# Optimization experiments

Measured on AMD Instinct MI355X. Metric: run time of the kernel, lower is better.

The kernel has to match this reference:

```python
import jax, jax.numpy as jnp
import numpy as np

B, T, D = 4, 4096, 1024
EPS = 1e-5


def _layernorm(x, w):
    mu = jnp.mean(x, axis=-1, keepdims=True)
    var = jnp.var(x, axis=-1, keepdims=True)
    return (x - mu) * jax.lax.rsqrt(var + EPS) * w


def setup_inputs() -> dict:
    key = jax.random.key(0)
    k0, k1, k2, k3 = jax.random.split(key, 4)
    x = jax.random.normal(k0, (B, T, D), dtype=jnp.float32)
    lengths = jax.random.randint(k1, (B,), 1, T + 1, dtype=jnp.int32)
    ln1_w = jnp.ones((D,), dtype=jnp.float32)
    ln2_w = jnp.ones((D,), dtype=jnp.float32)
    Wfc = jax.random.normal(k2, (D, 4 * D), dtype=jnp.float32) * 0.02
    Wproj = jax.random.normal(k3, (4 * D, D), dtype=jnp.float32) * 0.02
    return {"x": x, "lengths": lengths, "ln1_w": ln1_w, "ln2_w": ln2_w,
            "Wfc": Wfc, "Wproj": Wproj}


def reference(x, lengths, ln1_w, ln2_w, Wfc, Wproj):
    b, t, d = x.shape
    # valid[b, i] = i < lengths[b]  (non-padded positions)
    valid = (jnp.arange(t)[None, :] < lengths[:, None]).astype(x.dtype)  # (B,T)

    # --- FusedQueryAtt: out[b,i] = h[b,i] + valid_i * sum_{j<=i} valid_j * gelu(h[b,j])
    h = _layernorm(x, ln1_w)
    g = jax.nn.gelu(h, approximate=False) * valid[:, :, None]  # (B,T,D)
    attn_out = h + valid[:, :, None] * jnp.cumsum(g, axis=1)
    x = x + attn_out  # residual around attn

    # --- MLP (bias=False, dropout=0 in eval)
    h2 = _layernorm(x, ln2_w)
    mlp_out = jax.nn.gelu(h2 @ Wfc, approximate=False) @ Wproj
    return x + mlp_out
```

## Files before the change

### kernel.cpp

```cpp
#include <hip/hip_runtime.h>
#include <hip/hip_bf16.h>
#include <math.h>

#define B_SZ 4
#define T_SZ 4096
#define D_SZ 1024
#define H_SZ 4096
#define CHUNK 16
#define NCHUNK (T_SZ / CHUNK)
#define NSEG 8
#define SEGC (NCHUNK / NSEG)
#define LN_EPS 1e-5f

using frag8 = __attribute__((ext_vector_type(8))) short;
using f32x4 = __attribute__((ext_vector_type(4))) float;

__device__ __forceinline__ float gelu_exact(float x) {
  return 0.5f * x * (1.0f + erff(x * 0.70710678118654752f));
}

__device__ __forceinline__ float gelu_fast(float x) {
  float u2 = 1.5957691216057308f * (x + 0.044715f * x * x * x);
  float e = __expf(u2);
  return x - x * __builtin_amdgcn_rcpf(e + 1.0f);
}

__device__ __forceinline__ unsigned short f2bf(float f) {
  unsigned u = __float_as_uint(f);
  u += 0x7fffu + ((u >> 16) & 1u);
  return (unsigned short)(u >> 16);
}

__global__ __launch_bounds__(256) void attn_phase1(
    const float* __restrict__ x, const int* __restrict__ lengths,
    const float* __restrict__ w1, float* __restrict__ partial,
    float* __restrict__ csum) {
  __shared__ float red[8];
  int b = blockIdx.x >> 8;
  int c = blockIdx.x & (NCHUNK - 1);
  int tid = threadIdx.x;
  int len = lengths[b];
  float4 w = ((const float4*)w1)[tid];
  float run0 = 0.f, run1 = 0.f, run2 = 0.f, run3 = 0.f;
  for (int i = 0; i < CHUNK; ++i) {
    int t = c * CHUNK + i;
    size_t row = ((size_t)b * T_SZ + t) * D_SZ;
    float4 v = ((const float4*)(x + row))[tid];
    float s = v.x + v.y + v.z + v.w;
    float q = v.x * v.x + v.y * v.y + v.z * v.z + v.w * v.w;
#pragma unroll
    for (int o = 32; o > 0; o >>= 1) {
      s += __shfl_xor(s, o, 64);
      q += __shfl_xor(q, o, 64);
    }
    if ((tid & 63) == 0) { red[(tid >> 6) * 2] = s; red[(tid >> 6) * 2 + 1] = q; }
    __syncthreads();
    s = red[0] + red[2] + red[4] + red[6];
    q = red[1] + red[3] + red[5] + red[7];
    __syncthreads();
    float mu = s * (1.0f / D_SZ);
    float var = q * (1.0f / D_SZ) - mu * mu;
    float rstd = rsqrtf(var + LN_EPS);
    bool valid = t < len;
    float hx = (v.x - mu) * rstd * w.x, hy = (v.y - mu) * rstd * w.y;
    float hz = (v.z - mu) * rstd * w.z, hw = (v.w - mu) * rstd * w.w;
    if (valid) {
      run0 += gelu_exact(hx); run1 += gelu_exact(hy);
      run2 += gelu_exact(hz); run3 += gelu_exact(hw);
    }
    float4 p;
    p.x = v.x + hx + (valid ? run0 : 0.f);
    p.y = v.y + hy + (valid ? run1 : 0.f);
    p.z = v.z + hz + (valid ? run2 : 0.f);
    p.w = v.w + hw + (valid ? run3 : 0.f);
    ((float4*)(partial + row))[tid] = p;
  }
  float4 cs; cs.x = run0; cs.y = run1; cs.z = run2; cs.w = run3;
  ((float4*)(csum + ((size_t)b * NCHUNK + c) * D_SZ))[tid] = cs;
}

__global__ __launch_bounds__(256) void seg_scan(float* __restrict__ csum,
                                                float* __restrict__ segsum) {
  int blk = blockIdx.x;
  int b = blk >> 5, seg = (blk >> 2) & 7, dq = blk & 3;
  int d = dq * 256 + threadIdx.x;
  float* p = csum + ((size_t)b * NCHUNK + seg * SEGC) * D_SZ + d;
  float acc = 0.f;
#pragma unroll 8
  for (int j = 0; j < SEGC; ++j) {
    float v = p[(size_t)j * D_SZ];
    p[(size_t)j * D_SZ] = acc;
    acc += v;
  }
  segsum[((size_t)b * NSEG + seg) * D_SZ + d] = acc;
}

__global__ __launch_bounds__(256) void attn_phase2_ln2(
    float* __restrict__ xres, const float* __restrict__ csum,
    const float* __restrict__ segsum, const int* __restrict__ lengths,
    const float* __restrict__ w2, unsigned short* __restrict__ h2) {
  __shared__ float red[8];
  int t = blockIdx.x & (T_SZ - 1);
  int b = blockIdx.x >> 12;
  int tid = threadIdx.x;
  bool valid = t < lengths[b];
  int c = t / CHUNK;
  int seg = c >> 5;
  size_t row = ((size_t)b * T_SZ + t) * D_SZ;
  float4 v = ((const float4*)(xres + row))[tid];
  if (valid) {
    float4 o = ((const float4*)(csum + ((size_t)b * NCHUNK + c) * D_SZ))[tid];
    for (int s = 0; s < seg; ++s) {
      float4 g = ((const float4*)(segsum + ((size_t)b * NSEG + s) * D_SZ))[tid];
      o.x += g.x; o.y += g.y; o.z += g.z; o.w += g.w;
    }
    v.x += o.x; v.y += o.y; v.z += o.z; v.w += o.w;
  }
  ((float4*)(xres + row))[tid] = v;
  float s = v.x + v.y + v.z + v.w;
  float q = v.x * v.x + v.y * v.y + v.z * v.z + v.w * v.w;
#pragma unroll
  for (int o = 32; o > 0; o >>= 1) {
    s += __shfl_xor(s, o, 64);
    q += __shfl_xor(q, o, 64);
  }
  int wv = tid >> 6;
  if ((tid & 63) == 0) { red[wv * 2] = s; red[wv * 2 + 1] = q; }
  __syncthreads();
  s = red[0] + red[2] + red[4] + red[6];
  q = red[1] + red[3] + red[5] + red[7];
  float mu = s * (1.0f / D_SZ);
  float var = q * (1.0f / D_SZ) - mu * mu;
  float rstd = rsqrtf(var + LN_EPS);
  float4 w = ((const float4*)w2)[tid];
  ushort4 hq;
  hq.x = f2bf((v.x - mu) * rstd * w.x);
  hq.y = f2bf((v.y - mu) * rstd * w.y);
  hq.z = f2bf((v.z - mu) * rstd * w.z);
  hq.w = f2bf((v.w - mu) * rstd * w.w);
  ((ushort4*)(h2 + row))[tid] = hq;
}

__global__ __launch_bounds__(256) void transpose_f32_to_bf16(
    const float* __restrict__ src, unsigned short* __restrict__ dst,
    int R, int C) {
  __shared__ float tile[32][33];
  int bx = blockIdx.x * 32;
  int by = blockIdx.y * 32;
  int tx = threadIdx.x & 31;
  int ty = threadIdx.x >> 5;
#pragma unroll
  for (int i = 0; i < 32; i += 8)
    tile[ty + i][tx] = src[(size_t)(by + ty + i) * C + bx + tx];
  __syncthreads();
#pragma unroll
  for (int i = 0; i < 32; i += 8)
    dst[(size_t)(bx + ty + i) * R + by + tx] = f2bf(tile[tx][ty + i]);
}

#define GLD16(gsrc, ldsoff)                                                   \
  __builtin_amdgcn_global_load_lds(                                           \
      (const __attribute__((address_space(1))) unsigned int*)(gsrc),          \
      (__attribute__((address_space(3))) unsigned int*)(smc + (ldsoff)), 16,  \
      0, 0)

#define STAGE_A(P, k0e)                                                       \
  do {                                                                        \
    GLD16(gA + (size_t)0 * K + (k0e), aW + 0 + (P));                          \
    GLD16(gA + (size_t)32 * K + (k0e), aW + 4096 + (P));                      \
    GLD16(gA + (size_t)64 * K + (k0e), aW + 8192 + (P));                      \
    GLD16(gA + (size_t)96 * K + (k0e), aW + 12288 + (P));                     \
  } while (0)

#define STAGE_B(P, k0e)                                                       \
  do {                                                                        \
    GLD16(gB + (size_t)0 * K + (k0e), bW + 0 + (P));                          \
    GLD16(gB + (size_t)32 * K + (k0e), bW + 4096 + (P));                      \
    GLD16(gB + (size_t)64 * K + (k0e), bW + 8192 + (P));                      \
    GLD16(gB + (size_t)96 * K + (k0e), bW + 12288 + (P));                     \
  } while (0)

template <int P>
__device__ __forceinline__ void rd_af(const char* smc, int aB0, int aB1,
                                      frag8 (&af)[4][2]) {
#pragma unroll
  for (int tm = 0; tm < 4; ++tm) {
    af[tm][0] = *(const frag8*)(smc + aB0 + (P + tm * 2048));
    af[tm][1] = *(const frag8*)(smc + aB1 + (P + tm * 2048));
  }
}

template <int P>
__device__ __forceinline__ void rd_bf(const char* smc, int bB0, int bB1,
                                      frag8 (&bf)[4][2]) {
#pragma unroll
  for (int tn = 0; tn < 4; ++tn) {
    bf[tn][0] = *(const frag8*)(smc + bB0 + (P + tn * 2048));
    bf[tn][1] = *(const frag8*)(smc + bB1 + (P + tn * 2048));
  }
}

#define GBAR()                          \
  do {                                  \
    asm volatile("" ::: "memory");      \
    __builtin_amdgcn_s_barrier();       \
    asm volatile("" ::: "memory");      \
  } while (0)

#define TILE_BODY(t, P)                                                       \
  do {                                                                        \
    bool p1 = (t) + 1 < nt, p2 = (t) + 2 < nt;                                \
    rd_af<P>(smc, aB0, aB1, af);                                              \
    rd_bf<P>(smc, bB0, bB1, bf);                                              \
    asm volatile("s_waitcnt lgkmcnt(0)" ::: "memory");                        \
    GBAR();                                                                   \
    if (p2) {                                                                 \
      STAGE_A(P, ((t) + 2) * 64);                                             \
      STAGE_B(P, ((t) + 2) * 64);                                             \
    }                                                                         \
    __builtin_amdgcn_s_setprio(1);                                            \
    _Pragma("unroll") for (int kk = 0; kk < 2; ++kk)                          \
        _Pragma("unroll") for (int tm = 0; tm < 4; ++tm)                      \
            _Pragma("unroll") for (int tn = 0; tn < 4; ++tn)                  \
                acc[tm][tn] = __builtin_amdgcn_mfma_f32_16x16x32_bf16(        \
                    af[tm][kk], bf[tn][kk], acc[tm][tn], 0, 0, 0);            \
    __builtin_amdgcn_s_setprio(0);                                            \
    if (p2 && p1)                                                             \
      asm volatile("s_waitcnt vmcnt(8)" ::: "memory");                        \
    else                                                                      \
      asm volatile("s_waitcnt vmcnt(0)" ::: "memory");                        \
    GBAR();                                                                   \
  } while (0)

__global__ __launch_bounds__(256, 2) void gemm128_bt(
    const unsigned short* __restrict__ A, const unsigned short* __restrict__ Bt,
    int N, int K, int gx,
    const float* __restrict__ resid, float* __restrict__ outf,
    unsigned short* __restrict__ outb, int epi) {
  extern __shared__ char smc[];

  int orig = blockIdx.x, nwg = gridDim.x;
  int wg = orig;
  if ((nwg & 7) == 0) wg = (orig & 7) * (nwg >> 3) + (orig >> 3);
  int bx = wg % gx, by = wg / gx;
  int bm = by * 128, bn = bx * 128;

  int tid = threadIdx.x;
  int lane = tid & 63, wave = tid >> 6;
  int wm = wave >> 1, wn = wave & 1;
  int quad = lane >> 4, r16 = lane & 15;

  const unsigned short* A_blk = A + (size_t)bm * K;
  const unsigned short* B_blk = Bt + (size_t)bn * K;
  int nt = K >> 6;

  int swz = (r16 & 7) << 4;
  int aB0 = (wm * 64 + r16) * 128 + ((quad * 16) ^ swz);
  int aB1 = (wm * 64 + r16) * 128 + ((64 + quad * 16) ^ swz);
  int bB0 = 32768 + (wn * 64 + r16) * 128 + ((quad * 16) ^ swz);
  int bB1 = 32768 + (wn * 64 + r16) * 128 + ((64 + quad * 16) ^ swz);

  int arow = tid >> 3;
  int kc = ((tid & 7) * 8) ^ ((arow & 7) << 3);
  const unsigned short* gA = A_blk + (size_t)arow * K + kc;
  const unsigned short* gB = B_blk + (size_t)arow * K + kc;
  int aW = arow * 128 + (tid & 7) * 16;
  int bW = 32768 + arow * 128 + (tid & 7) * 16;

  f32x4 acc[4][4] = {};
  frag8 af[4][2], bf[4][2];

  STAGE_A(0, 0);
  STAGE_B(0, 0);
  if (nt > 1) {
    STAGE_A(16384, 64);
    STAGE_B(16384, 64);
    asm volatile("s_waitcnt vmcnt(8)" ::: "memory");
  } else {
    asm volatile("s_waitcnt vmcnt(0)" ::: "memory");
  }
  GBAR();

  for (int t = 0; t < nt; t += 2) {
    TILE_BODY(t, 0);
    TILE_BODY(t + 1, 16384);
  }

  if (epi == 0) {
#pragma unroll
    for (int tm = 0; tm < 4; ++tm) {
#pragma unroll
      for (int tn = 0; tn < 4; ++tn) {
        int gm0 = bm + wm * 64 + tm * 16 + quad * 4;
        int gn = bn + wn * 64 + tn * 16 + r16;
#pragma unroll
        for (int r = 0; r < 4; ++r)
          outb[(size_t)(gm0 + r) * N + gn] = f2bf(gelu_fast(acc[tm][tn][r]));
      }
    }
  } else {
#pragma unroll
    for (int tm = 0; tm < 4; ++tm) {
#pragma unroll
      for (int tn = 0; tn < 4; ++tn) {
        int gm0 = bm + wm * 64 + tm * 16 + quad * 4;
        int gn = bn + wn * 64 + tn * 16 + r16;
#pragma unroll
        for (int r = 0; r < 4; ++r)
          outf[(size_t)(gm0 + r) * N + gn] =
              resid[(size_t)(gm0 + r) * N + gn] + acc[tm][tn][r];
      }
    }
  }
}

extern "C" void kernel_launch(void* const* d_in, const int* in_sizes, int n_in,
                              void* d_out, int out_size, void* d_ws,
                              size_t ws_size, hipStream_t stream) {
  const float* x = (const float*)d_in[0];
  const int* lengths = (const int*)d_in[1];
  const float* ln1_w = (const float*)d_in[2];
  const float* ln2_w = (const float*)d_in[3];
  const float* Wfc = (const float*)d_in[4];
  const float* Wproj = (const float*)d_in[5];
  float* out = (float*)d_out;

  static bool lds_cfg = false;
  if (!lds_cfg) {
    hipFuncSetAttribute((const void*)gemm128_bt,
                        hipFuncAttributeMaxDynamicSharedMemorySize, 65536);
    lds_cfg = true;
  }

  char* ws = (char*)d_ws;
  size_t off = 0;
  float* segsum = (float*)(ws + off);
  off += (size_t)B_SZ * NSEG * D_SZ * sizeof(float);
  float* csum = (float*)(ws + off);
  off += (size_t)B_SZ * NCHUNK * D_SZ * sizeof(float);
  unsigned short* wfcb = (unsigned short*)(ws + off);
  off += (size_t)D_SZ * H_SZ * sizeof(unsigned short);
  unsigned short* wprojb = (unsigned short*)(ws + off);
  off += (size_t)H_SZ * D_SZ * sizeof(unsigned short);
  unsigned short* h2 = (unsigned short*)(ws + off);
  off += (size_t)B_SZ * T_SZ * D_SZ * sizeof(unsigned short);
  unsigned short* act = (unsigned short*)(ws + off);

  const int M = B_SZ * T_SZ;
  const size_t tileBytes = 256ull * H_SZ * sizeof(unsigned short);
  size_t avail = (ws_size > off) ? (ws_size - off) : 0;
  int sliceTiles = (int)(avail / tileBytes);
  if (sliceTiles < 1) sliceTiles = 1;
  int sliceM = sliceTiles * 256;
  if (sliceM > M) sliceM = M;

  attn_phase1<<<B_SZ * NCHUNK, 256, 0, stream>>>(x, lengths, ln1_w, out, csum);
  seg_scan<<<B_SZ * NSEG * (D_SZ / 256), 256, 0, stream>>>(csum, segsum);
  attn_phase2_ln2<<<B_SZ * T_SZ, 256, 0, stream>>>(out, csum, segsum, lengths,
                                                   ln2_w, h2);
  transpose_f32_to_bf16<<<dim3(H_SZ / 32, D_SZ / 32), 256, 0, stream>>>(
      Wfc, wfcb, D_SZ, H_SZ);
  transpose_f32_to_bf16<<<dim3(D_SZ / 32, H_SZ / 32), 256, 0, stream>>>(
      Wproj, wprojb, H_SZ, D_SZ);

  for (int m0 = 0; m0 < M; m0 += sliceM) {
    int rows = (M - m0 < sliceM) ? (M - m0) : sliceM;
    int rb = rows / 128;
    gemm128_bt<<<dim3((H_SZ / 128) * rb), 256, 65536, stream>>>(
        h2 + (size_t)m0 * D_SZ, wfcb, H_SZ, D_SZ, H_SZ / 128,
        nullptr, nullptr, act, 0);
    gemm128_bt<<<dim3((D_SZ / 128) * rb), 256, 65536, stream>>>(
        act, wprojb, D_SZ, H_SZ, D_SZ / 128,
        out + (size_t)m0 * D_SZ, out + (size_t)m0 * D_SZ, nullptr, 1);
  }
}
```

Before: 481.5 us.

## Use 256x256 GEMM tiles with A fragments loaded directly from global into registers

The MLP GEMM changes from 128x128 tiles on 256 threads to 256x256 tiles on 512 threads (8 waves in a 2x4 layout). Only the B operand is still staged through LDS via global_load_lds. Each wave loads its A fragments straight from global memory into registers, prefetching the next k-step's A between MFMA groups. The goal is higher arithmetic intensity per block and less LDS traffic and fewer barriers, at the cost of more registers (8x4 accumulators plus 16 A fragments), a full vmcnt(0) wait each step, and uncoalesced-ish direct A loads.

```diff
diff --git a/kernel.cpp b/kernel.cpp
--- a/kernel.cpp
+++ b/kernel.cpp
@@ -164,41 +164,13 @@
       (__attribute__((address_space(3))) unsigned int*)(smc + (ldsoff)), 16,  \
       0, 0)
 
-#define STAGE_A(P, k0e)                                                       \
-  do {                                                                        \
-    GLD16(gA + (size_t)0 * K + (k0e), aW + 0 + (P));                          \
-    GLD16(gA + (size_t)32 * K + (k0e), aW + 4096 + (P));                      \
-    GLD16(gA + (size_t)64 * K + (k0e), aW + 8192 + (P));                      \
-    GLD16(gA + (size_t)96 * K + (k0e), aW + 12288 + (P));                     \
-  } while (0)
-
 #define STAGE_B(P, k0e)                                                       \
   do {                                                                        \
     GLD16(gB + (size_t)0 * K + (k0e), bW + 0 + (P));                          \
-    GLD16(gB + (size_t)32 * K + (k0e), bW + 4096 + (P));                      \
     GLD16(gB + (size_t)64 * K + (k0e), bW + 8192 + (P));                      \
-    GLD16(gB + (size_t)96 * K + (k0e), bW + 12288 + (P));                     \
+    GLD16(gB + (size_t)128 * K + (k0e), bW + 16384 + (P));                    \
+    GLD16(gB + (size_t)192 * K + (k0e), bW + 24576 + (P));                    \
   } while (0)
-
-template <int P>
-__device__ __forceinline__ void rd_af(const char* smc, int aB0, int aB1,
-                                      frag8 (&af)[4][2]) {
-#pragma unroll
-  for (int tm = 0; tm < 4; ++tm) {
-    af[tm][0] = *(const frag8*)(smc + aB0 + (P + tm * 2048));
-    af[tm][1] = *(const frag8*)(smc + aB1 + (P + tm * 2048));
-  }
-}
-
-template <int P>
-__device__ __forceinline__ void rd_bf(const char* smc, int bB0, int bB1,
-                                      frag8 (&bf)[4][2]) {
-#pragma unroll
-  for (int tn = 0; tn < 4; ++tn) {
-    bf[tn][0] = *(const frag8*)(smc + bB0 + (P + tn * 2048));
-    bf[tn][1] = *(const frag8*)(smc + bB1 + (P + tn * 2048));
-  }
-}
 
 #define GBAR()                          \
   do {                                  \
@@ -210,29 +182,30 @@
 #define TILE_BODY(t, P)                                                       \
   do {                                                                        \
     bool p1 = (t) + 1 < nt, p2 = (t) + 2 < nt;                                \
-    rd_af<P>(smc, aB0, aB1, af);                                              \
-    rd_bf<P>(smc, bB0, bB1, bf);                                              \
+    asm volatile("s_waitcnt vmcnt(0)" ::: "memory");                          \
+    _Pragma("unroll") for (int tn = 0; tn < 4; ++tn) {                        \
+      bf[tn][0] = *(const frag8*)(smc + bB0 + ((P) + tn * 2048));             \
+      bf[tn][1] = *(const frag8*)(smc + bB1 + ((P) + tn * 2048));             \
+    }                                                                         \
     asm volatile("s_waitcnt lgkmcnt(0)" ::: "memory");                        \
     GBAR();                                                                   \
-    if (p2) {                                                                 \
-      STAGE_A(P, ((t) + 2) * 64);                                             \
-      STAGE_B(P, ((t) + 2) * 64);                                             \
+    if (p2) STAGE_B(P, ((t) + 2) * 64);                                       \
+    const char* aNxt = aBase + (size_t)((t) + 1) * 128;                       \
+    _Pragma("unroll") for (int tm = 0; tm < 8; ++tm) {                        \
+      __builtin_amdgcn_s_setprio(1);                                          \
+      _Pragma("unroll") for (int kk = 0; kk < 2; ++kk)                        \
+          _Pragma("unroll") for (int tn = 0; tn < 4; ++tn)                    \
+              acc[tm][tn] = __builtin_amdgcn_mfma_f32_16x16x32_bf16(          \
+                  af[tm][kk], bf[tn][kk], acc[tm][tn], 0, 0, 0);              \
+      __builtin_amdgcn_s_setprio(0);                                          \
+      if (p1) {                                                               \
+        af[tm][0] = *(const frag8*)(aNxt + aOff[tm]);                         \
+        af[tm][1] = *(const frag8*)(aNxt + aOff[tm] + 64);                    \
+      }                                                                       \
     }                                                                         \
-    __builtin_amdgcn_s_setprio(1);                                            \
-    _Pragma("unroll") for (int kk = 0; kk < 2; ++kk)                          \
-        _Pragma("unroll") for (int tm = 0; tm < 4; ++tm)                      \
-            _Pragma("unroll") for (int tn = 0; tn < 4; ++tn)                  \
-                acc[tm][tn] = __builtin_amdgcn_mfma_f32_16x16x32_bf16(        \
-                    af[tm][kk], bf[tn][kk], acc[tm][tn], 0, 0, 0);            \
-    __builtin_amdgcn_s_setprio(0);                                            \
-    if (p2 && p1)                                                             \
-      asm volatile("s_waitcnt vmcnt(8)" ::: "memory");                        \
-    else                                                                      \
-      asm volatile("s_waitcnt vmcnt(0)" ::: "memory");                        \
-    GBAR();                                                                   \
   } while (0)
 
-__global__ __launch_bounds__(256, 2) void gemm128_bt(
+__global__ __launch_bounds__(512, 2) void gemm256_ar(
     const unsigned short* __restrict__ A, const unsigned short* __restrict__ Bt,
     int N, int K, int gx,
     const float* __restrict__ resid, float* __restrict__ outf,
@@ -243,11 +216,11 @@
   int wg = orig;
   if ((nwg & 7) == 0) wg = (orig & 7) * (nwg >> 3) + (orig >> 3);
   int bx = wg % gx, by = wg / gx;
-  int bm = by * 128, bn = bx * 128;
+  int bm = by * 256, bn = bx * 256;
 
   int tid = threadIdx.x;
   int lane = tid & 63, wave = tid >> 6;
-  int wm = wave >> 1, wn = wave & 1;
+  int wm = wave >> 2, wn = wave & 3;
   int quad = lane >> 4, r16 = lane & 15;
 
   const unsigned short* A_blk = A + (size_t)bm * K;
@@ -255,43 +228,45 @@
   int nt = K >> 6;
 
   int swz = (r16 & 7) << 4;
-  int aB0 = (wm * 64 + r16) * 128 + ((quad * 16) ^ swz);
-  int aB1 = (wm * 64 + r16) * 128 + ((64 + quad * 16) ^ swz);
-  int bB0 = 32768 + (wn * 64 + r16) * 128 + ((quad * 16) ^ swz);
-  int bB1 = 32768 + (wn * 64 + r16) * 128 + ((64 + quad * 16) ^ swz);
-
-  int arow = tid >> 3;
-  int kc = ((tid & 7) * 8) ^ ((arow & 7) << 3);
-  const unsigned short* gA = A_blk + (size_t)arow * K + kc;
-  const unsigned short* gB = B_blk + (size_t)arow * K + kc;
-  int aW = arow * 128 + (tid & 7) * 16;
-  int bW = 32768 + arow * 128 + (tid & 7) * 16;
-
-  f32x4 acc[4][4] = {};
-  frag8 af[4][2], bf[4][2];
-
-  STAGE_A(0, 0);
+  int bB0 = (wn * 64 + r16) * 128 + ((quad * 16) ^ swz);
+  int bB1 = (wn * 64 + r16) * 128 + ((64 + quad * 16) ^ swz);
+
+  int brow = tid >> 3;
+  int kc = ((tid & 7) * 8) ^ ((brow & 7) << 3);
+  const unsigned short* gB = B_blk + (size_t)brow * K + kc;
+  int bW = brow * 128 + (tid & 7) * 16;
+
+  const char* aBase = (const char*)A_blk;
+  int aOff[8];
+#pragma unroll
+  for (int tm = 0; tm < 8; ++tm)
+    aOff[tm] = (((wm * 128 + tm * 16 + r16) * K) + quad * 8) * 2;
+
+  f32x4 acc[8][4] = {};
+  frag8 af[8][2];
+  frag8 bf[4][2];
+
   STAGE_B(0, 0);
-  if (nt > 1) {
-    STAGE_A(16384, 64);
-    STAGE_B(16384, 64);
-    asm volatile("s_waitcnt vmcnt(8)" ::: "memory");
-  } else {
-    asm volatile("s_waitcnt vmcnt(0)" ::: "memory");
-  }
+  if (nt > 1) STAGE_B(32768, 64);
+#pragma unroll
+  for (int tm = 0; tm < 8; ++tm) {
+    af[tm][0] = *(const frag8*)(aBase + aOff[tm]);
+    af[tm][1] = *(const frag8*)(aBase + aOff[tm] + 64);
+  }
+  asm volatile("s_waitcnt vmcnt(0)" ::: "memory");
   GBAR();
 
   for (int t = 0; t < nt; t += 2) {
     TILE_BODY(t, 0);
-    TILE_BODY(t + 1, 16384);
+    TILE_BODY(t + 1, 32768);
   }
 
   if (epi == 0) {
 #pragma unroll
-    for (int tm = 0; tm < 4; ++tm) {
+    for (int tm = 0; tm < 8; ++tm) {
 #pragma unroll
       for (int tn = 0; tn < 4; ++tn) {
-        int gm0 = bm + wm * 64 + tm * 16 + quad * 4;
+        int gm0 = bm + wm * 128 + tm * 16 + quad * 4;
         int gn = bn + wn * 64 + tn * 16 + r16;
 #pragma unroll
         for (int r = 0; r < 4; ++r)
@@ -300,10 +275,10 @@
     }
   } else {
 #pragma unroll
-    for (int tm = 0; tm < 4; ++tm) {
+    for (int tm = 0; tm < 8; ++tm) {
 #pragma unroll
       for (int tn = 0; tn < 4; ++tn) {
-        int gm0 = bm + wm * 64 + tm * 16 + quad * 4;
+        int gm0 = bm + wm * 128 + tm * 16 + quad * 4;
         int gn = bn + wn * 64 + tn * 16 + r16;
 #pragma unroll
         for (int r = 0; r < 4; ++r)
@@ -327,7 +302,7 @@
 
   static bool lds_cfg = false;
   if (!lds_cfg) {
-    hipFuncSetAttribute((const void*)gemm128_bt,
+    hipFuncSetAttribute((const void*)gemm256_ar,
                         hipFuncAttributeMaxDynamicSharedMemorySize, 65536);
     lds_cfg = true;
   }
@@ -365,12 +340,12 @@
 
   for (int m0 = 0; m0 < M; m0 += sliceM) {
     int rows = (M - m0 < sliceM) ? (M - m0) : sliceM;
-    int rb = rows / 128;
-    gemm128_bt<<<dim3((H_SZ / 128) * rb), 256, 65536, stream>>>(
-        h2 + (size_t)m0 * D_SZ, wfcb, H_SZ, D_SZ, H_SZ / 128,
+    int r1 = rows / 256;
+    gemm256_ar<<<dim3((H_SZ / 256) * r1), 512, 65536, stream>>>(
+        h2 + (size_t)m0 * D_SZ, wfcb, H_SZ, D_SZ, H_SZ / 256,
         nullptr, nullptr, act, 0);
-    gemm128_bt<<<dim3((D_SZ / 128) * rb), 256, 65536, stream>>>(
-        act, wprojb, D_SZ, H_SZ, D_SZ / 128,
+    gemm256_ar<<<dim3((D_SZ / 256) * r1), 512, 65536, stream>>>(
+        act, wprojb, D_SZ, H_SZ, D_SZ / 256,
         out + (size_t)m0 * D_SZ, out + (size_t)m0 * D_SZ, nullptr, 1);
   }
 }
```

Result: slower. 823.2 us (+71.0%).
